# Kernel tuning notes

Hardware: AMD Instinct MI355X
Metric: run time of the kernel (lower is better)

## Reference

```python
import jax, jax.numpy as jnp
import numpy as np

C = 512
GROUPS = 32
EPS = 1e-6


def group_norm(x, gamma, beta):
    # x: [B,C,H,W]
    b, c, h, w = x.shape
    xg = x.reshape(b, GROUPS, c // GROUPS, h, w)
    mean = xg.mean(axis=(2, 3, 4), keepdims=True)
    var = xg.var(axis=(2, 3, 4), keepdims=True)
    xg = (xg - mean) / jnp.sqrt(var + EPS)
    xn = xg.reshape(b, c, h, w)
    return xn * gamma[None, :, None, None] + beta[None, :, None, None]


def conv1x1(x, w, bias):
    # x: [B,C,H,W], w: [Cout,Cin], bias: [Cout]
    return jnp.einsum('bchw,dc->bdhw', x, w) + bias[None, :, None, None]


def setup_inputs() -> dict:
    key = jax.random.key(0)
    ks = jax.random.split(key, 10)
    scale = 1.0 / np.sqrt(C)
    return {
        'x': jax.random.normal(ks[0], (4, C, 64, 64), dtype=jnp.float32),
        'gn_gamma': jnp.ones((C,), jnp.float32),
        'gn_beta': jnp.zeros((C,), jnp.float32),
        'wq': jax.random.normal(ks[1], (C, C), jnp.float32) * scale,
        'bq': jnp.zeros((C,), jnp.float32),
        'wk': jax.random.normal(ks[2], (C, C), jnp.float32) * scale,
        'bk': jnp.zeros((C,), jnp.float32),
        'wv': jax.random.normal(ks[3], (C, C), jnp.float32) * scale,
        'bv': jnp.zeros((C,), jnp.float32),
        'wp': jax.random.normal(ks[4], (C, C), jnp.float32) * scale,
        'bp': jnp.zeros((C,), jnp.float32),
    }


def reference(x, gn_gamma, gn_beta, wq, bq, wk, bk, wv, bv, wp, bp):
    b, c, h, w = x.shape
    h_ = group_norm(x, gn_gamma, gn_beta)
    q = conv1x1(h_, wq, bq).reshape(b, c, h * w)  # [B,C,N]
    k = conv1x1(h_, wk, bk).reshape(b, c, h * w)
    v = conv1x1(h_, wv, bv).reshape(b, c, h * w)
    # attn[b,i,j] = softmax_j(q_i . k_j / sqrt(c))
    attn = jnp.einsum('bci,bcj->bij', q, k) * (c ** -0.5)  # [B,N,N]
    attn = jax.nn.softmax(attn, axis=2)
    a = jnp.einsum('bij,bcj->bci', attn, v).reshape(b, c, h, w)
    a = conv1x1(a, wp, bp)
    return x + a
```

## Files before the change

kernel.cpp:

```cpp
#include <hip/hip_runtime.h>
#include <hip/hip_bf16.h>

#define B_ 4
#define C_ 512
#define N_ 4096
#define G_ 32
#define CPG_ 16

typedef __bf16 bf16;
using bf16x4 = __attribute__((ext_vector_type(4))) __bf16;
using bf16x8 = __attribute__((ext_vector_type(8))) __bf16;
using f32x4  = __attribute__((ext_vector_type(4))) float;

__global__ __launch_bounds__(256) void gn_stats(const float* __restrict__ x,
                                                float* __restrict__ mv,
                                                float* __restrict__ rv) {
    __shared__ float r1[4], r2[4];
    const int bg = blockIdx.x;
    const float* xg = x + (long)bg * (CPG_ * N_);
    const int tid = threadIdx.x;
    float s = 0.f, ss = 0.f;
    for (int i = tid; i < CPG_ * N_ / 4; i += 256) {
        f32x4 v = ((const f32x4*)xg)[i];
#pragma unroll
        for (int j = 0; j < 4; ++j) { s += v[j]; ss += v[j] * v[j]; }
    }
#pragma unroll
    for (int o = 32; o > 0; o >>= 1) { s += __shfl_down(s, o); ss += __shfl_down(ss, o); }
    if ((tid & 63) == 0) { r1[tid >> 6] = s; r2[tid >> 6] = ss; }
    __syncthreads();
    if (tid == 0) {
        float S = r1[0] + r1[1] + r1[2] + r1[3];
        float SS = r2[0] + r2[1] + r2[2] + r2[3];
        float mean = S / (CPG_ * N_);
        float var = SS / (CPG_ * N_) - mean * mean;
        mv[bg] = mean;
        rv[bg] = rsqrtf(var + 1e-6f);
    }
}

__global__ __launch_bounds__(256) void gn_apply(const float* __restrict__ x,
                                                const float* __restrict__ mv,
                                                const float* __restrict__ rv,
                                                const float* __restrict__ gamma,
                                                const float* __restrict__ beta,
                                                bf16* __restrict__ ht) {
    __shared__ float tile[64][65];
    const int b = blockIdx.z, c0 = blockIdx.y * 64, n0 = blockIdx.x * 64;
    const int tid = threadIdx.x;
    const int rr = tid >> 4, cc4 = (tid & 15) * 4;
    const float* xb = x + ((long)b * C_ + c0) * N_ + n0;
#pragma unroll
    for (int p2 = 0; p2 < 4; ++p2) {
        const int cl = p2 * 16 + rr;
        const int g = (c0 + cl) >> 4;
        const float m = mv[b * G_ + g], rs = rv[b * G_ + g];
        const float ga = gamma[c0 + cl], be = beta[c0 + cl];
        f32x4 v = *(const f32x4*)&xb[(long)cl * N_ + cc4];
#pragma unroll
        for (int j = 0; j < 4; ++j) tile[cl][cc4 + j] = (v[j] - m) * rs * ga + be;
    }
    __syncthreads();
    bf16* hb = ht + ((long)b * N_ + n0) * C_ + c0;
#pragma unroll
    for (int p2 = 0; p2 < 4; ++p2) {
        const int nn = p2 * 16 + rr;
        bf16x4 o4 = { (bf16)tile[cc4 + 0][nn], (bf16)tile[cc4 + 1][nn],
                      (bf16)tile[cc4 + 2][nn], (bf16)tile[cc4 + 3][nn] };
        *(bf16x4*)&hb[(long)nn * C_ + cc4] = o4;
    }
}

__global__ __launch_bounds__(256) void f2b4(const float* __restrict__ w0, const float* __restrict__ w1,
                                            const float* __restrict__ w2, const float* __restrict__ w3,
                                            bf16* __restrict__ o0, bf16* __restrict__ o1,
                                            bf16* __restrict__ o2, bf16* __restrict__ o3, int n4) {
    const float* in = (blockIdx.y == 0) ? w0 : (blockIdx.y == 1) ? w1 : (blockIdx.y == 2) ? w2 : w3;
    bf16* o = (blockIdx.y == 0) ? o0 : (blockIdx.y == 1) ? o1 : (blockIdx.y == 2) ? o2 : o3;
    int i = blockIdx.x * 256 + threadIdx.x;
    if (i < n4) {
        f32x4 v = ((const f32x4*)in)[i];
        bf16x4 r = { (bf16)v[0], (bf16)v[1], (bf16)v[2], (bf16)v[3] };
        ((bf16x4*)o)[i] = r;
    }
}

template <int OUTF32, int BIASMODE , int RESID, int GRIDSWAP>
__global__ __launch_bounds__(256, 2)
void gemm_bt(const bf16* __restrict__ A, const bf16* __restrict__ Bt,
             void* __restrict__ outp, const float* __restrict__ bias,
             const float* __restrict__ resid,
             int M, int N, int K, float scale,
             long aStride, long btStride, long outStride, long residStride) {
    __shared__ __align__(16) bf16 lA[128 * 32];
    __shared__ __align__(16) bf16 lB[128 * 32];

    const int tid = threadIdx.x;
    const int wid = tid >> 6;
    const int lane = tid & 63;
    const int z = blockIdx.z;
    A += (long)z * aStride;
    Bt += (long)z * btStride;
    const int bm = (GRIDSWAP ? blockIdx.x : blockIdx.y) * 128;
    const int bn = (GRIDSWAP ? blockIdx.y : blockIdx.x) * 128;
    const int wr = (wid >> 1) * 64;
    const int wc = (wid & 1) * 64;

    f32x4 acc[4][4];
#pragma unroll
    for (int m = 0; m < 4; ++m)
#pragma unroll
        for (int n = 0; n < 4; ++n) acc[m][n] = (f32x4){0.f, 0.f, 0.f, 0.f};

    const int srow = lane >> 2;
    const int skcol = (lane & 3) * 8;
    const int lr = lane >> 4;
    const int lc = lane & 15;

    for (int k0 = 0; k0 < K; k0 += 32) {
#pragma unroll
        for (int c = 0; c < 2; ++c) {
            const int chunk = wid * 2 + c;
            const int row = chunk * 16 + srow;
            const bf16* gA = A + (long)(bm + row) * K + (k0 + skcol);
            const bf16* gB = Bt + (long)(bn + row) * K + (k0 + skcol);
            __builtin_amdgcn_global_load_lds(
                (const __attribute__((address_space(1))) void*)gA,
                (__attribute__((address_space(3))) void*)&lA[chunk * 512], 16, 0, 0);
            __builtin_amdgcn_global_load_lds(
                (const __attribute__((address_space(1))) void*)gB,
                (__attribute__((address_space(3))) void*)&lB[chunk * 512], 16, 0, 0);
        }
        __syncthreads();
        bf16x8 aF[4], bF[4];
#pragma unroll
        for (int m = 0; m < 4; ++m)
            aF[m] = *(const bf16x8*)&lA[(wr + m * 16 + lc) * 32 + lr * 8];
#pragma unroll
        for (int n = 0; n < 4; ++n)
            bF[n] = *(const bf16x8*)&lB[(wc + n * 16 + lc) * 32 + lr * 8];
#pragma unroll
        for (int m = 0; m < 4; ++m)
#pragma unroll
            for (int n = 0; n < 4; ++n)
                acc[m][n] = __builtin_amdgcn_mfma_f32_16x16x32_bf16(aF[m], bF[n],
                                                                    acc[m][n], 0, 0, 0);
        __syncthreads();
    }

    float* outF = (float*)outp + (long)z * outStride;
    bf16* outB = (bf16*)outp + (long)z * outStride;
    const float* res = resid + (long)z * residStride;
#pragma unroll
    for (int m = 0; m < 4; ++m) {
#pragma unroll
        for (int n = 0; n < 4; ++n) {
            const int gc = bn + wc + n * 16 + lc;
            float cb = (BIASMODE == 1) ? bias[gc] : 0.f;
#pragma unroll
            for (int j = 0; j < 4; ++j) {
                const int gr = bm + wr + m * 16 + lr * 4 + j;
                float v = acc[m][n][j] * scale + cb;
                if (BIASMODE == 2) v += bias[gr];
                long idx = (long)gr * N + gc;
                if (RESID) v += res[idx];
                if (OUTF32) outF[idx] = v;
                else        outB[idx] = (bf16)v;
            }
        }
    }
}

__global__ __launch_bounds__(256) void softmax_b16(bf16* __restrict__ sc) {
    __shared__ float red[4];
    const long row = blockIdx.x;
    const int tid = threadIdx.x;
    bf16* pr = sc + row * N_;
    bf16x8 v0 = ((bf16x8*)pr)[tid];
    bf16x8 v1 = ((bf16x8*)pr)[tid + 256];
    float f[16];
#pragma unroll
    for (int j = 0; j < 8; ++j) { f[j] = (float)v0[j]; f[8 + j] = (float)v1[j]; }
    float mx = -1e30f;
#pragma unroll
    for (int j = 0; j < 16; ++j) mx = fmaxf(mx, f[j]);
#pragma unroll
    for (int o = 32; o > 0; o >>= 1) mx = fmaxf(mx, __shfl_down(mx, o));
    if ((tid & 63) == 0) red[tid >> 6] = mx;
    __syncthreads();
    mx = fmaxf(fmaxf(red[0], red[1]), fmaxf(red[2], red[3]));
    float sum = 0.f;
#pragma unroll
    for (int j = 0; j < 16; ++j) { f[j] = __expf(f[j] - mx); sum += f[j]; }
#pragma unroll
    for (int o = 32; o > 0; o >>= 1) sum += __shfl_down(sum, o);
    __syncthreads();
    if ((tid & 63) == 0) red[tid >> 6] = sum;
    __syncthreads();
    const float inv = 1.f / (red[0] + red[1] + red[2] + red[3]);
#pragma unroll
    for (int j = 0; j < 8; ++j) {
        v0[j] = (bf16)(f[j] * inv);
        v1[j] = (bf16)(f[8 + j] * inv);
    }
    ((bf16x8*)pr)[tid] = v0;
    ((bf16x8*)pr)[tid + 256] = v1;
}

extern "C" void kernel_launch(void* const* d_in, const int* in_sizes, int n_in,
                              void* d_out, int out_size, void* d_ws, size_t ws_size,
                              hipStream_t stream) {
    const float* x     = (const float*)d_in[0];
    const float* gamma = (const float*)d_in[1];
    const float* beta  = (const float*)d_in[2];
    const float* wq = (const float*)d_in[3]; const float* bq = (const float*)d_in[4];
    const float* wk = (const float*)d_in[5]; const float* bk = (const float*)d_in[6];
    const float* wv = (const float*)d_in[7]; const float* bv = (const float*)d_in[8];
    const float* wp = (const float*)d_in[9]; const float* bp = (const float*)d_in[10];

    char* w = (char*)d_ws;
    size_t off = 0;
    auto take = [&](size_t bytes) -> void* {
        void* pp = w + off;
        off += (bytes + 255) & ~(size_t)255;
        return pp;
    };
    float* mv = (float*)take(B_ * G_ * 4);
    float* rv = (float*)take(B_ * G_ * 4);
    bf16* wqb = (bf16*)take((size_t)C_ * C_ * 2);
    bf16* wkb = (bf16*)take((size_t)C_ * C_ * 2);
    bf16* wvb = (bf16*)take((size_t)C_ * C_ * 2);
    bf16* wpb = (bf16*)take((size_t)C_ * C_ * 2);
    bf16* ht  = (bf16*)take((size_t)B_ * N_ * C_ * 2);
    bf16* qt  = (bf16*)take((size_t)B_ * N_ * C_ * 2);
    bf16* kt  = (bf16*)take((size_t)B_ * N_ * C_ * 2);
    bf16* vv  = (bf16*)take((size_t)B_ * C_ * N_ * 2);
    bf16* at  = ht;

    const bool tierA = ws_size >= 203424768ULL;

    gn_stats<<<dim3(B_ * G_), 256, 0, stream>>>(x, mv, rv);
    gn_apply<<<dim3(N_ / 64, C_ / 64, B_), 256, 0, stream>>>(x, mv, rv, gamma, beta, ht);
    f2b4<<<dim3(C_ * C_ / 4 / 256, 4), 256, 0, stream>>>(wq, wk, wv, wp, wqb, wkb, wvb, wpb,
                                                         C_ * C_ / 4);

    gemm_bt<0, 1, 0, 1><<<dim3(B_ * N_ / 128, C_ / 128, 1), 256, 0, stream>>>(
        ht, wqb, qt, bq, nullptr, B_ * N_, C_, C_, 1.f, 0, 0, 0, 0);
    gemm_bt<0, 1, 0, 1><<<dim3(B_ * N_ / 128, C_ / 128, 1), 256, 0, stream>>>(
        ht, wkb, kt, bk, nullptr, B_ * N_, C_, C_, 1.f, 0, 0, 0, 0);
    gemm_bt<0, 2, 0, 0><<<dim3(N_ / 128, C_ / 128, B_), 256, 0, stream>>>(
        wvb, ht, vv, bv, nullptr, C_, N_, C_, 1.f, 0, (long)N_ * C_, (long)C_ * N_, 0);

    const float scl = 0.044194173824159216f;
    if (tierA) {
        bf16* sc = (bf16*)take((size_t)B_ * N_ * N_ * 2);
        gemm_bt<0, 0, 0, 0><<<dim3(N_ / 128, N_ / 128, B_), 256, 0, stream>>>(
            qt, kt, sc, nullptr, nullptr, N_, N_, C_, scl,
            (long)N_ * C_, (long)N_ * C_, (long)N_ * N_, 0);
        softmax_b16<<<dim3(B_ * N_), 256, 0, stream>>>(sc);
        gemm_bt<0, 0, 0, 1><<<dim3(N_ / 128, C_ / 128, B_), 256, 0, stream>>>(
            sc, vv, at, nullptr, nullptr, N_, C_, N_, 1.f,
            (long)N_ * N_, (long)C_ * N_, (long)N_ * C_, 0);
    } else {
        bf16* sc = (bf16*)take((size_t)2 * N_ * N_ * 2);
        for (int p = 0; p < 2; ++p) {
            const long o2 = (long)p * 2 * N_ * C_;
            gemm_bt<0, 0, 0, 0><<<dim3(N_ / 128, N_ / 128, 2), 256, 0, stream>>>(
                qt + o2, kt + o2, sc, nullptr, nullptr, N_, N_, C_, scl,
                (long)N_ * C_, (long)N_ * C_, (long)N_ * N_, 0);
            softmax_b16<<<dim3(2 * N_), 256, 0, stream>>>(sc);
            gemm_bt<0, 0, 0, 1><<<dim3(N_ / 128, C_ / 128, 2), 256, 0, stream>>>(
                sc, vv + o2, at + o2, nullptr, nullptr, N_, C_, N_, 1.f,
                (long)N_ * N_, (long)C_ * N_, (long)N_ * C_, 0);
        }
    }
    gemm_bt<1, 2, 1, 0><<<dim3(N_ / 128, C_ / 128, B_), 256, 0, stream>>>(
        wpb, at, d_out, bp, x, C_, N_, C_, 1.f, 0, (long)N_ * C_,
        (long)C_ * N_, (long)C_ * N_);
}
```

Baseline: 424.0 us.

## Fuse softmax exp into QK GEMM epilogue and defer normalization to PV GEMM

```diff
diff --git a/kernel.cpp b/kernel.cpp
--- a/kernel.cpp
+++ b/kernel.cpp
@@ -85,11 +85,15 @@
     }
 }
 
-template <int OUTF32, int BIASMODE , int RESID, int GRIDSWAP>
+template <int OUTF32, int BIASMODE , int RESID, int GRIDSWAP,
+          int EXPSUM, int INVSUM, int DUAL>
 __global__ __launch_bounds__(256, 2)
 void gemm_bt(const bf16* __restrict__ A, const bf16* __restrict__ Bt,
              void* __restrict__ outp, const float* __restrict__ bias,
              const float* __restrict__ resid,
+             float* __restrict__ rowpart, const float* __restrict__ invsum,
+             const bf16* __restrict__ Bt2, const float* __restrict__ bias2,
+             void* __restrict__ outp2,
              int M, int N, int K, float scale,
              long aStride, long btStride, long outStride, long residStride) {
     __shared__ __align__(16) bf16 lA[128 * 32];
@@ -101,8 +105,13 @@
     const int z = blockIdx.z;
     A += (long)z * aStride;
     Bt += (long)z * btStride;
+    int ybn = GRIDSWAP ? blockIdx.y : blockIdx.x;
+    if (DUAL) {
+        const int half = gridDim.y >> 1;
+        if (ybn >= half) { ybn -= half; Bt = Bt2; bias = bias2; outp = outp2; }
+    }
     const int bm = (GRIDSWAP ? blockIdx.x : blockIdx.y) * 128;
-    const int bn = (GRIDSWAP ? blockIdx.y : blockIdx.x) * 128;
+    const int bn = ybn * 128;
     const int wr = (wid >> 1) * 64;
     const int wc = (wid & 1) * 64;
 
@@ -148,6 +157,58 @@
         __syncthreads();
     }
 
+    if constexpr (EXPSUM) {
+        __shared__ float rsum[2][128];
+        bf16* outB = (bf16*)outp + (long)z * outStride;
+        float s_mj[4][4];
+#pragma unroll
+        for (int m = 0; m < 4; ++m)
+#pragma unroll
+            for (int j = 0; j < 4; ++j) s_mj[m][j] = 0.f;
+#pragma unroll
+        for (int m = 0; m < 4; ++m)
+#pragma unroll
+            for (int n = 0; n < 4; ++n) {
+                const int gc = bn + wc + n * 16 + lc;
+#pragma unroll
+                for (int j = 0; j < 4; ++j) {
+                    const int gr = bm + wr + m * 16 + lr * 4 + j;
+                    float e = __expf(fminf(acc[m][n][j] * scale, 60.f));
+                    outB[(long)gr * N + gc] = (bf16)e;
+                    s_mj[m][j] += e;
+                }
+            }
+#pragma unroll
+        for (int m = 0; m < 4; ++m)
+#pragma unroll
+            for (int j = 0; j < 4; ++j)
+#pragma unroll
+                for (int o = 1; o < 16; o <<= 1)
+                    s_mj[m][j] += __shfl_xor(s_mj[m][j], o);
+        if (lc == 0) {
+#pragma unroll
+            for (int m = 0; m < 4; ++m)
+#pragma unroll
+                for (int j = 0; j < 4; ++j)
+                    rsum[wc >> 6][wr + m * 16 + lr * 4 + j] = s_mj[m][j];
+        }
+        __syncthreads();
+        if (tid < 128) {
+            float p = rsum[0][tid] + rsum[1][tid];
+            rowpart[((long)z * M + bm + tid) * gridDim.x + blockIdx.x] = p;
+        }
+        return;
+    }
+
+    float invs[4][4];
+    if constexpr (INVSUM) {
+#pragma unroll
+        for (int m = 0; m < 4; ++m)
+#pragma unroll
+            for (int j = 0; j < 4; ++j)
+                invs[m][j] = invsum[(long)z * M + bm + wr + m * 16 + lr * 4 + j];
+    }
+
     float* outF = (float*)outp + (long)z * outStride;
     bf16* outB = (bf16*)outp + (long)z * outStride;
     const float* res = resid + (long)z * residStride;
@@ -160,7 +221,8 @@
 #pragma unroll
             for (int j = 0; j < 4; ++j) {
                 const int gr = bm + wr + m * 16 + lr * 4 + j;
-                float v = acc[m][n][j] * scale + cb;
+                float v = INVSUM ? acc[m][n][j] * invs[m][j]
+                                 : acc[m][n][j] * scale + cb;
                 if (BIASMODE == 2) v += bias[gr];
                 long idx = (long)gr * N + gc;
                 if (RESID) v += res[idx];
@@ -171,40 +233,13 @@
     }
 }
 
-__global__ __launch_bounds__(256) void softmax_b16(bf16* __restrict__ sc) {
-    __shared__ float red[4];
-    const long row = blockIdx.x;
-    const int tid = threadIdx.x;
-    bf16* pr = sc + row * N_;
-    bf16x8 v0 = ((bf16x8*)pr)[tid];
-    bf16x8 v1 = ((bf16x8*)pr)[tid + 256];
-    float f[16];
-#pragma unroll
-    for (int j = 0; j < 8; ++j) { f[j] = (float)v0[j]; f[8 + j] = (float)v1[j]; }
-    float mx = -1e30f;
-#pragma unroll
-    for (int j = 0; j < 16; ++j) mx = fmaxf(mx, f[j]);
-#pragma unroll
-    for (int o = 32; o > 0; o >>= 1) mx = fmaxf(mx, __shfl_down(mx, o));
-    if ((tid & 63) == 0) red[tid >> 6] = mx;
-    __syncthreads();
-    mx = fmaxf(fmaxf(red[0], red[1]), fmaxf(red[2], red[3]));
-    float sum = 0.f;
-#pragma unroll
-    for (int j = 0; j < 16; ++j) { f[j] = __expf(f[j] - mx); sum += f[j]; }
-#pragma unroll
-    for (int o = 32; o > 0; o >>= 1) sum += __shfl_down(sum, o);
-    __syncthreads();
-    if ((tid & 63) == 0) red[tid >> 6] = sum;
-    __syncthreads();
-    const float inv = 1.f / (red[0] + red[1] + red[2] + red[3]);
-#pragma unroll
-    for (int j = 0; j < 8; ++j) {
-        v0[j] = (bf16)(f[j] * inv);
-        v1[j] = (bf16)(f[8 + j] * inv);
-    }
-    ((bf16x8*)pr)[tid] = v0;
-    ((bf16x8*)pr)[tid + 256] = v1;
+__global__ __launch_bounds__(256) void rowinv(const float* __restrict__ rowpart,
+                                              float* __restrict__ invsum, int nblk) {
+    const int row = blockIdx.x * 256 + threadIdx.x;
+    const float* rp = rowpart + (long)row * nblk;
+    float s = 0.f;
+    for (int i = 0; i < nblk; ++i) s += rp[i];
+    invsum[row] = 1.f / s;
 }
 
 extern "C" void kernel_launch(void* const* d_in, const int* in_sizes, int n_in,
@@ -236,45 +271,49 @@
     bf16* kt  = (bf16*)take((size_t)B_ * N_ * C_ * 2);
     bf16* vv  = (bf16*)take((size_t)B_ * C_ * N_ * 2);
     bf16* at  = ht;
-
-    const bool tierA = ws_size >= 203424768ULL;
+    float* rowpart = (float*)take((size_t)B_ * N_ * 32 * 4);
+    float* invsum  = (float*)take((size_t)B_ * N_ * 4);
+
+    const bool tierA = ws_size >= 205587456ULL;
 
     gn_stats<<<dim3(B_ * G_), 256, 0, stream>>>(x, mv, rv);
     gn_apply<<<dim3(N_ / 64, C_ / 64, B_), 256, 0, stream>>>(x, mv, rv, gamma, beta, ht);
     f2b4<<<dim3(C_ * C_ / 4 / 256, 4), 256, 0, stream>>>(wq, wk, wv, wp, wqb, wkb, wvb, wpb,
                                                          C_ * C_ / 4);
 
-    gemm_bt<0, 1, 0, 1><<<dim3(B_ * N_ / 128, C_ / 128, 1), 256, 0, stream>>>(
-        ht, wqb, qt, bq, nullptr, B_ * N_, C_, C_, 1.f, 0, 0, 0, 0);
-    gemm_bt<0, 1, 0, 1><<<dim3(B_ * N_ / 128, C_ / 128, 1), 256, 0, stream>>>(
-        ht, wkb, kt, bk, nullptr, B_ * N_, C_, C_, 1.f, 0, 0, 0, 0);
-    gemm_bt<0, 2, 0, 0><<<dim3(N_ / 128, C_ / 128, B_), 256, 0, stream>>>(
-        wvb, ht, vv, bv, nullptr, C_, N_, C_, 1.f, 0, (long)N_ * C_, (long)C_ * N_, 0);
+    gemm_bt<0, 1, 0, 1, 0, 0, 1><<<dim3(B_ * N_ / 128, 2 * C_ / 128, 1), 256, 0, stream>>>(
+        ht, wqb, qt, bq, nullptr, nullptr, nullptr, wkb, bk, kt,
+        B_ * N_, C_, C_, 1.f, 0, 0, 0, 0);
+    gemm_bt<0, 2, 0, 0, 0, 0, 0><<<dim3(N_ / 128, C_ / 128, B_), 256, 0, stream>>>(
+        wvb, ht, vv, bv, nullptr, nullptr, nullptr, nullptr, nullptr, nullptr,
+        C_, N_, C_, 1.f, 0, (long)N_ * C_, (long)C_ * N_, 0);
 
     const float scl = 0.044194173824159216f;
     if (tierA) {
         bf16* sc = (bf16*)take((size_t)B_ * N_ * N_ * 2);
-        gemm_bt<0, 0, 0, 0><<<dim3(N_ / 128, N_ / 128, B_), 256, 0, stream>>>(
-            qt, kt, sc, nullptr, nullptr, N_, N_, C_, scl,
-            (long)N_ * C_, (long)N_ * C_, (long)N_ * N_, 0);
-        softmax_b16<<<dim3(B_ * N_), 256, 0, stream>>>(sc);
-        gemm_bt<0, 0, 0, 1><<<dim3(N_ / 128, C_ / 128, B_), 256, 0, stream>>>(
-            sc, vv, at, nullptr, nullptr, N_, C_, N_, 1.f,
-            (long)N_ * N_, (long)C_ * N_, (long)N_ * C_, 0);
+        gemm_bt<0, 0, 0, 0, 1, 0, 0><<<dim3(N_ / 128, N_ / 128, B_), 256, 0, stream>>>(
+            qt, kt, sc, nullptr, nullptr, rowpart, nullptr, nullptr, nullptr, nullptr,
+            N_, N_, C_, scl, (long)N_ * C_, (long)N_ * C_, (long)N_ * N_, 0);
+        rowinv<<<dim3(B_ * N_ / 256), 256, 0, stream>>>(rowpart, invsum, N_ / 128);
+        gemm_bt<0, 0, 0, 1, 0, 1, 0><<<dim3(N_ / 128, C_ / 128, B_), 256, 0, stream>>>(
+            sc, vv, at, nullptr, nullptr, nullptr, invsum, nullptr, nullptr, nullptr,
+            N_, C_, N_, 1.f, (long)N_ * N_, (long)C_ * N_, (long)N_ * C_, 0);
     } else {
         bf16* sc = (bf16*)take((size_t)2 * N_ * N_ * 2);
         for (int p = 0; p < 2; ++p) {
             const long o2 = (long)p * 2 * N_ * C_;
-            gemm_bt<0, 0, 0, 0><<<dim3(N_ / 128, N_ / 128, 2), 256, 0, stream>>>(
-                qt + o2, kt + o2, sc, nullptr, nullptr, N_, N_, C_, scl,
+            gemm_bt<0, 0, 0, 0, 1, 0, 0><<<dim3(N_ / 128, N_ / 128, 2), 256, 0, stream>>>(
+                qt + o2, kt + o2, sc, nullptr, nullptr, rowpart, nullptr, nullptr,
+                nullptr, nullptr, N_, N_, C_, scl,
                 (long)N_ * C_, (long)N_ * C_, (long)N_ * N_, 0);
-            softmax_b16<<<dim3(2 * N_), 256, 0, stream>>>(sc);
-            gemm_bt<0, 0, 0, 1><<<dim3(N_ / 128, C_ / 128, 2), 256, 0, stream>>>(
-                sc, vv + o2, at + o2, nullptr, nullptr, N_, C_, N_, 1.f,
+            rowinv<<<dim3(2 * N_ / 256), 256, 0, stream>>>(rowpart, invsum, N_ / 128);
+            gemm_bt<0, 0, 0, 1, 0, 1, 0><<<dim3(N_ / 128, C_ / 128, 2), 256, 0, stream>>>(
+                sc, vv + o2, at + o2, nullptr, nullptr, nullptr, invsum, nullptr,
+                nullptr, nullptr, N_, C_, N_, 1.f,
                 (long)N_ * N_, (long)C_ * N_, (long)N_ * C_, 0);
         }
     }
-    gemm_bt<1, 2, 1, 0><<<dim3(N_ / 128, C_ / 128, B_), 256, 0, stream>>>(
-        wpb, at, d_out, bp, x, C_, N_, C_, 1.f, 0, (long)N_ * C_,
-        (long)C_ * N_, (long)C_ * N_);
-}
+    gemm_bt<1, 2, 1, 0, 0, 0, 0><<<dim3(N_ / 128, C_ / 128, B_), 256, 0, stream>>>(
+        wpb, at, d_out, bp, x, nullptr, nullptr, nullptr, nullptr, nullptr,
+        C_, N_, C_, 1.f, 0, (long)N_ * C_, (long)C_ * N_, (long)C_ * N_);
+}
```

Result: faster. 390.2 us (-8.0%).
